# Kernel tuning notes

Measured on AMD Instinct MI355X. Metric: run time of the kernel, lower is better.

Reference implementation:

```python
import jax, jax.numpy as jnp
import numpy as np

N = 65536   # total nodes (B graphs * PG nodes)
B = 4096    # number of session graphs in batch
PG = 16     # nodes per graph
D = 128     # embedding_dim (= GRU hidden = attn hidden)
MAXD = 8    # max in-degree (mailbox length)
EPS = 1e-5  # BatchNorm eps


def _bn(x, gamma, beta, mean, var):
    # eval-mode BatchNorm1d
    return (x - mean) * (gamma / jnp.sqrt(var + EPS)) + beta


def _gru_cell(m, h, w_ih, w_hh, b_ih, b_hh):
    # torch.nn.GRU cell math; m,h: [N,D]
    gi = m @ w_ih.T + b_ih
    gh = h @ w_hh.T + b_hh
    i_r, i_z, i_n = jnp.split(gi, 3, axis=-1)
    h_r, h_z, h_n = jnp.split(gh, 3, axis=-1)
    r = jax.nn.sigmoid(i_r + h_r)
    z = jax.nn.sigmoid(i_z + h_z)
    n = jnp.tanh(i_n + r * h_n)
    return (1.0 - z) * n + z * h


def _forward(feat, intend, position_weight,
             bn1_gamma, bn1_beta, bn1_mean, bn1_var,
             gru_w_ih, gru_w_hh, gru_b_ih, gru_b_hh,
             fc_self_w, fc_neigh_w, prelu_a,
             bn2_gamma, bn2_beta, bn2_mean, bn2_var,
             fc_u_w, fc_v_w, fc_v_b, fc_i_w, fc_i_b, fc_e_w,
             last_nodes, edge_src, edge_dst, edge_slot, seg_ids):
    # ---- EOPA: copy_u messages -> per-node GRU over mailbox -> final hidden ----
    x = _bn(feat, bn1_gamma, bn1_beta, bn1_mean, bn1_var)
    mailbox = jnp.zeros((N, MAXD, D), x.dtype).at[edge_dst, edge_slot].set(x[edge_src])
    mask = jnp.zeros((N, MAXD), bool).at[edge_dst, edge_slot].set(True)

    def step(h, inp):
        m_t, mk_t = inp  # [N,D], [N]
        h_new = _gru_cell(m_t, h, gru_w_ih, gru_w_hh, gru_b_ih, gru_b_hh)
        return jnp.where(mk_t[:, None], h_new, h), None

    h0 = jnp.zeros((N, D), x.dtype)
    neigh, _ = jax.lax.scan(step, h0, (mailbox.transpose(1, 0, 2), mask.T))
    rst = x @ fc_self_w.T + neigh @ fc_neigh_w.T
    rst = jnp.where(rst > 0, rst, prelu_a * rst)  # PReLU(embedding_dim)

    # ---- AttnReadout: segment softmax attention + position-weighted readout ----
    f = _bn(rst, bn2_gamma, bn2_beta, bn2_mean, bn2_var)
    feat_u = f @ fc_u_w.T                                  # [N,D]
    feat_v = (intend @ fc_v_w.T + fc_v_b)[seg_ids]         # broadcast_nodes
    feat_l = (f[last_nodes] @ fc_i_w.T + fc_i_b)[seg_ids]  # broadcast_nodes
    e = (jax.nn.sigmoid(feat_u + feat_v + feat_l) @ fc_e_w.T)[:, 0]  # [N]
    # segment softmax over graphs
    e_max = jax.ops.segment_max(e, seg_ids, num_segments=B)
    e_exp = jnp.exp(e - e_max[seg_ids])
    denom = jax.ops.segment_sum(e_exp, seg_ids, num_segments=B)
    alpha = e_exp / denom[seg_ids]
    rst_g = jax.ops.segment_sum(f * alpha[:, None], seg_ids, num_segments=B)
    pos_g = jax.ops.segment_sum(f * position_weight[:, None], seg_ids, num_segments=B)
    return rst_g, pos_g


def setup_inputs() -> dict:
    rng = np.random.default_rng(0)
    deg = rng.integers(1, 5, size=N)                    # in-degree 1..4 <= MAXD
    E = int(deg.sum())
    edge_dst = np.repeat(np.arange(N), deg).astype(np.int32)
    starts = np.concatenate([[0], np.cumsum(deg)[:-1]])
    edge_slot = (np.arange(E) - np.repeat(starts, deg)).astype(np.int32)
    graph_of = (np.arange(N) // PG).astype(np.int32)
    edge_src = (graph_of[edge_dst].astype(np.int64) * PG
                + rng.integers(0, PG, size=E)).astype(np.int32)
    last_nodes = (np.arange(B) * PG + PG - 1).astype(np.int32)

    key = jax.random.key(0)
    ks = jax.random.split(key, 20)
    s = 0.05
    nrm = lambda k, sh, sc=s: jax.random.normal(k, sh, dtype=jnp.float32) * sc
    return dict(
        feat=nrm(ks[0], (N, D), 1.0),
        intend=nrm(ks[1], (B, D), 1.0),
        position_weight=jax.random.uniform(ks[2], (N,), dtype=jnp.float32),
        bn1_gamma=jnp.ones((D,), jnp.float32), bn1_beta=jnp.zeros((D,), jnp.float32),
        bn1_mean=nrm(ks[3], (D,)), bn1_var=jnp.ones((D,), jnp.float32),
        gru_w_ih=nrm(ks[4], (3 * D, D)), gru_w_hh=nrm(ks[5], (3 * D, D)),
        gru_b_ih=nrm(ks[6], (3 * D,)), gru_b_hh=nrm(ks[7], (3 * D,)),
        fc_self_w=nrm(ks[8], (D, D)), fc_neigh_w=nrm(ks[9], (D, D)),
        prelu_a=jnp.full((D,), 0.25, jnp.float32),
        bn2_gamma=jnp.ones((D,), jnp.float32), bn2_beta=jnp.zeros((D,), jnp.float32),
        bn2_mean=nrm(ks[10], (D,)), bn2_var=jnp.ones((D,), jnp.float32),
        fc_u_w=nrm(ks[11], (D, D)), fc_v_w=nrm(ks[12], (D, D)), fc_v_b=nrm(ks[13], (D,)),
        fc_i_w=nrm(ks[14], (D, D)), fc_i_b=nrm(ks[15], (D,)),
        fc_e_w=nrm(ks[16], (1, D)),
        last_nodes=jnp.asarray(last_nodes),
        edge_src=jnp.asarray(edge_src), edge_dst=jnp.asarray(edge_dst),
        edge_slot=jnp.asarray(edge_slot), seg_ids=jnp.asarray(graph_of),
    )


def reference(feat, intend, position_weight,
              bn1_gamma, bn1_beta, bn1_mean, bn1_var,
              gru_w_ih, gru_w_hh, gru_b_ih, gru_b_hh,
              fc_self_w, fc_neigh_w, prelu_a,
              bn2_gamma, bn2_beta, bn2_mean, bn2_var,
              fc_u_w, fc_v_w, fc_v_b, fc_i_w, fc_i_b, fc_e_w,
              last_nodes, edge_src, edge_dst, edge_slot, seg_ids):
    return _forward(feat, intend, position_weight,
                    bn1_gamma, bn1_beta, bn1_mean, bn1_var,
                    gru_w_ih, gru_w_hh, gru_b_ih, gru_b_hh,
                    fc_self_w, fc_neigh_w, prelu_a,
                    bn2_gamma, bn2_beta, bn2_mean, bn2_var,
                    fc_u_w, fc_v_w, fc_v_b, fc_i_w, fc_i_b, fc_e_w,
                    last_nodes, edge_src, edge_dst, edge_slot, seg_ids)
```

## Files before the change

kernel.cpp:

```cpp
#include <hip/hip_runtime.h>
#include <math.h>

#define D 128
#define MAXD 8
#define EPSV 1e-5f

#define NODES 32
#define NI 2

typedef __attribute__((ext_vector_type(8))) short short8;
typedef __attribute__((ext_vector_type(4))) float f32x4;
typedef unsigned short ushort_t;

#define XH_OFF     0
#define RZ_OFF     8192
#define RZ_STRIDE  132
#define NP_OFF     25088
#define NP_STRIDE  68
#define X2_OFF     NP_OFF
#define F_OFF      RZ_OFF
#define SBIG_BYTES 33792

__device__ __forceinline__ float fast_rcp(float x) { return __builtin_amdgcn_rcpf(x); }
__device__ __forceinline__ float sigmoid_f(float x) {
    return fast_rcp(1.0f + __expf(-x));
}
__device__ __forceinline__ float tanh_f(float x) {
    return 1.0f - 2.0f * fast_rcp(1.0f + __expf(2.0f * x));
}
__device__ __forceinline__ ushort_t f2bf(float f) {
    unsigned int b = __float_as_uint(f);
    b += 0x7FFFu + ((b >> 16) & 1u);
    return (ushort_t)(b >> 16);
}
__device__ __forceinline__ float bf2f(ushort_t u) {
    return __uint_as_float(((unsigned int)u) << 16);
}

__global__ void prep_kernel(const float* __restrict__ wih, const float* __restrict__ whh,
                            const float* __restrict__ fs,  const float* __restrict__ fn,
                            const float* __restrict__ fu,  const float* __restrict__ fv,
                            const float* __restrict__ fi,
                            const float* __restrict__ g1, const float* __restrict__ b1,
                            const float* __restrict__ m1, const float* __restrict__ v1,
                            ushort_t* __restrict__ wih_bf, ushort_t* __restrict__ whh_bf,
                            ushort_t* __restrict__ fcs_bf, ushort_t* __restrict__ fcn_bf,
                            ushort_t* __restrict__ fcu_bf, ushort_t* __restrict__ fcv_bf,
                            ushort_t* __restrict__ fci_bf,
                            float* __restrict__ bn1sc, float* __restrict__ bn1sh) {
    int i = blockIdx.x * blockDim.x + threadIdx.x;
    if (i < 3 * D * D) {
        wih_bf[i] = f2bf(wih[i]);
        whh_bf[i] = f2bf(whh[i]);
    }
    if (i < D * D) {
        fcs_bf[i] = f2bf(fs[i]);
        fcn_bf[i] = f2bf(fn[i]);
        fcu_bf[i] = f2bf(fu[i]);
        fcv_bf[i] = f2bf(fv[i]);
        fci_bf[i] = f2bf(fi[i]);
    }
    if (i < D) {
        float sc = g1[i] * rsqrtf(v1[i] + EPSV);
        bn1sc[i] = sc;
        bn1sh[i] = b1[i] - m1[i] * sc;
    }
}

__global__ void mbinit_kernel(int* __restrict__ mb, int n) {
    int i = blockIdx.x * blockDim.x + threadIdx.x;
    if (i < n) mb[i] = -1;
}
__global__ void scatter_kernel(const int* __restrict__ src, const int* __restrict__ dst,
                               const int* __restrict__ slot, int* __restrict__ mb, int E) {
    int e = blockIdx.x * blockDim.x + threadIdx.x;
    if (e < E) mb[(size_t)dst[e] * MAXD + slot[e]] = src[e];
}

__device__ __forceinline__ void stage_bn1(const float* __restrict__ feat,
                                          const float* __restrict__ bn1sc,
                                          const float* __restrict__ bn1sh,
                                          int node0, int tid, char* dst) {
    int row = tid >> 4, u = tid & 15;
    const float4* fp = (const float4*)(feat + (size_t)(node0 + row) * D + u * 8);
    const float4* scp = (const float4*)(bn1sc + u * 8);
    const float4* shp = (const float4*)(bn1sh + u * 8);
    float4 f0 = fp[0], f1 = fp[1];
    float4 s0 = scp[0], s1 = scp[1];
    float4 h0 = shp[0], h1 = shp[1];
    unsigned int w0 = (unsigned int)f2bf(f0.x * s0.x + h0.x) | ((unsigned int)f2bf(f0.y * s0.y + h0.y) << 16);
    unsigned int w1 = (unsigned int)f2bf(f0.z * s0.z + h0.z) | ((unsigned int)f2bf(f0.w * s0.w + h0.w) << 16);
    unsigned int w2 = (unsigned int)f2bf(f1.x * s1.x + h1.x) | ((unsigned int)f2bf(f1.y * s1.y + h1.y) << 16);
    unsigned int w3 = (unsigned int)f2bf(f1.z * s1.z + h1.z) | ((unsigned int)f2bf(f1.w * s1.w + h1.w) << 16);
    *(uint4*)(dst + row * 256 + ((u ^ (row & 7)) << 4)) = make_uint4(w0, w1, w2, w3);
}

__global__ __launch_bounds__(512, 2) void mega_kernel(
        const float* __restrict__ feat, const int* __restrict__ mb,
        const ushort_t* __restrict__ wih_bf, const ushort_t* __restrict__ whh_bf,
        const float* __restrict__ gbih, const float* __restrict__ gbhh,
        const ushort_t* __restrict__ fcs_bf, const ushort_t* __restrict__ fcn_bf,
        const float* __restrict__ prelu,
        const float* __restrict__ bg, const float* __restrict__ bb,
        const float* __restrict__ bm, const float* __restrict__ bv,
        const ushort_t* __restrict__ fcu_bf, const ushort_t* __restrict__ fcv_bf,
        const ushort_t* __restrict__ fci_bf,
        const float* __restrict__ fvbias, const float* __restrict__ fibias,
        const float* __restrict__ fce,
        const float* __restrict__ intend, const float* __restrict__ pw,
        const float* __restrict__ bn1sc, const float* __restrict__ bn1sh,
        float* __restrict__ outp, int Bn) {
    __shared__ __align__(16) char sBig[SBIG_BYTES];
    __shared__ int   sSrcT[MAXD][36];
    __shared__ float sE[NODES][9];
    __shared__ float sAlpha[NODES];
    __shared__ float sPw[NODES];
    __shared__ int   sTmax;

    const int tid = threadIdx.x;
    const int w = tid >> 6;
    const int lane = tid & 63;
    const int lc = lane & 15;
    const int lg = lane >> 4;
    const int c = w * 16 + lc;
    const int node0 = blockIdx.x * NODES;
    const int g0 = blockIdx.x * (NODES / 16);

    const int swzc = c >> 3;
    const int clo = (c & 7) * 2;

    if (tid == 0) sTmax = 0;
    stage_bn1(feat, bn1sc, bn1sh, node0, tid, sBig + XH_OFF);
    if (tid < NODES * MAXD) {
        int rr = tid >> 3, ss = tid & 7;
        int s = mb[(size_t)(node0 + rr) * MAXD + ss];
        sSrcT[ss][rr] = (s >= 0) ? (s - node0) : -1;
    }
    if (tid < NODES) sPw[tid] = pw[node0 + tid];
    __syncthreads();
    if (tid < NODES) {
        int d = 0;
#pragma unroll
        for (int t = 0; t < MAXD; ++t)
            if (sSrcT[t][tid] >= 0) d = t + 1;
        atomicMax(&sTmax, d);
    }

    {
        short8 bIW[3][4];
#pragma unroll
        for (int g = 0; g < 3; ++g)
#pragma unroll
            for (int kf = 0; kf < 4; ++kf)
                bIW[g][kf] = *(const short8*)(wih_bf + (size_t)(g * D + c) * D + kf * 32 + lg * 8);
        const float bi0 = gbih[c], bi1 = gbih[D + c], bi2 = gbih[2 * D + c];

#pragma unroll
        for (int i = 0; i < NI; ++i) {
            int xrow = i * 16 + lc;
            short8 aF[4];
#pragma unroll
            for (int kf = 0; kf < 4; ++kf)
                aF[kf] = *(const short8*)(sBig + XH_OFF + xrow * 256 + (((kf * 4 + lg) ^ (xrow & 7)) << 4));
            f32x4 aR = {0.f, 0.f, 0.f, 0.f}, aZ = aR, aN = aR;
#pragma unroll
            for (int kf = 0; kf < 4; ++kf) {
                aR = __builtin_amdgcn_mfma_f32_16x16x32_bf16(aF[kf], bIW[0][kf], aR, 0, 0, 0);
                aZ = __builtin_amdgcn_mfma_f32_16x16x32_bf16(aF[kf], bIW[1][kf], aZ, 0, 0, 0);
                aN = __builtin_amdgcn_mfma_f32_16x16x32_bf16(aF[kf], bIW[2][kf], aN, 0, 0, 0);
            }
#pragma unroll
            for (int p = 0; p < 4; ++p) {
                int row = i * 16 + lg * 4 + p;
                unsigned int rz = (unsigned int)f2bf(aR[p] + bi0)
                                | ((unsigned int)f2bf(aZ[p] + bi1) << 16);
                *(unsigned int*)(sBig + RZ_OFF + c * RZ_STRIDE + row * 4) = rz;
                *(ushort_t*)(sBig + NP_OFF + c * NP_STRIDE + row * 2) = f2bf(aN[p] + bi2);
            }
            __builtin_amdgcn_sched_barrier(0);
        }
    }
    __syncthreads();

    const int Tmax = (sTmax > 0) ? sTmax : 1;
    short8 bHW[3][4];
#pragma unroll
    for (int g = 0; g < 3; ++g)
#pragma unroll
        for (int kf = 0; kf < 4; ++kf)
            bHW[g][kf] = *(const short8*)(whh_bf + (size_t)(g * D + c) * D + kf * 32 + lg * 8);
    const float bhr = gbhh[c], bhz = gbhh[D + c], bhn = gbhh[2 * D + c];

    for (int t = 0; t < Tmax; ++t) {
        unsigned int houts[NI][2];
#pragma unroll
        for (int i = 0; i < NI; ++i) {
            f32x4 aR = {0.f, 0.f, 0.f, 0.f}, aZ = aR, aHN = aR;
            if (t != 0) {
                int hrow = i * 16 + lc;
                short8 aF[4];
#pragma unroll
                for (int kf = 0; kf < 4; ++kf)
                    aF[kf] = *(const short8*)(sBig + XH_OFF + hrow * 256 + (((kf * 4 + lg) ^ (hrow & 7)) << 4));
#pragma unroll
                for (int kf = 0; kf < 4; ++kf) {
                    aR  = __builtin_amdgcn_mfma_f32_16x16x32_bf16(aF[kf], bHW[0][kf], aR, 0, 0, 0);
                    aZ  = __builtin_amdgcn_mfma_f32_16x16x32_bf16(aF[kf], bHW[1][kf], aZ, 0, 0, 0);
                    aHN = __builtin_amdgcn_mfma_f32_16x16x32_bf16(aF[kf], bHW[2][kf], aHN, 0, 0, 0);
                }
            }
#pragma unroll
            for (int p = 0; p < 4; ++p) {
                int row = i * 16 + lg * 4 + p;
                int srow = sSrcT[t][row];
                int act = srow >= 0;
                int gr = act ? srow : 0;
                unsigned int rz = *(const unsigned int*)(sBig + RZ_OFF + c * RZ_STRIDE + gr * 4);
                float gir = bf2f((ushort_t)(rz & 0xffffu));
                float giz = bf2f((ushort_t)(rz >> 16));
                float gin = bf2f(*(const ushort_t*)(sBig + NP_OFF + c * NP_STRIDE + gr * 2));
                float hold = 0.0f;
                if (t != 0)
                    hold = bf2f(*(const ushort_t*)(sBig + XH_OFF + row * 256 + ((swzc ^ (row & 7)) << 4) + clo));
                float r = sigmoid_f(gir + aR[p] + bhr);
                float z = sigmoid_f(giz + aZ[p] + bhz);
                float n = tanh_f(gin + r * (aHN[p] + bhn));
                float hv = (1.0f - z) * n + z * hold;
                hv = act ? hv : hold;
                unsigned int hb = (unsigned int)f2bf(hv);
                if (p & 1) houts[i][p >> 1] |= hb << 16;
                else       houts[i][p >> 1]  = hb;
            }
            __builtin_amdgcn_sched_barrier(0);
        }
        __syncthreads();
#pragma unroll
        for (int i = 0; i < NI; ++i)
#pragma unroll
            for (int p = 0; p < 4; ++p) {
                int row = i * 16 + lg * 4 + p;
                ushort_t hb = (ushort_t)((houts[i][p >> 1] >> ((p & 1) * 16)) & 0xffffu);
                *(ushort_t*)(sBig + XH_OFF + row * 256 + ((swzc ^ (row & 7)) << 4) + clo) = hb;
            }
        __syncthreads();
    }

    stage_bn1(feat, bn1sc, bn1sh, node0, tid, sBig + X2_OFF);
    __syncthreads();
    {
        const float pa = prelu[c];
        const float s2 = bg[c] * rsqrtf(bv[c] + EPSV);
        const float h2 = bb[c] - bm[c] * s2;
        const ushort_t* fcs_c = fcs_bf + (size_t)c * D + lg * 8;
        const ushort_t* fcn_c = fcn_bf + (size_t)c * D + lg * 8;
#pragma unroll
        for (int i = 0; i < NI; ++i) {
            int xrow = i * 16 + lc;
            f32x4 a = {0.f, 0.f, 0.f, 0.f};
            {
                short8 xA[4];
#pragma unroll
                for (int kf = 0; kf < 4; ++kf)
                    xA[kf] = *(const short8*)(sBig + X2_OFF + xrow * 256 + (((kf * 4 + lg) ^ (xrow & 7)) << 4));
#pragma unroll
                for (int kf = 0; kf < 4; ++kf)
                    a = __builtin_amdgcn_mfma_f32_16x16x32_bf16(xA[kf], *(const short8*)(fcs_c + kf * 32), a, 0, 0, 0);
            }
            {
                short8 hA[4];
#pragma unroll
                for (int kf = 0; kf < 4; ++kf)
                    hA[kf] = *(const short8*)(sBig + XH_OFF + xrow * 256 + (((kf * 4 + lg) ^ (xrow & 7)) << 4));
#pragma unroll
                for (int kf = 0; kf < 4; ++kf)
                    a = __builtin_amdgcn_mfma_f32_16x16x32_bf16(hA[kf], *(const short8*)(fcn_c + kf * 32), a, 0, 0, 0);
            }
#pragma unroll
            for (int p = 0; p < 4; ++p) {
                int row = i * 16 + lg * 4 + p;
                float v = a[p];
                v = v > 0.0f ? v : pa * v;
                v = v * s2 + h2;
                *(ushort_t*)(sBig + F_OFF + row * 256 + ((swzc ^ (row & 7)) << 4) + clo) = f2bf(v);
            }
            __builtin_amdgcn_sched_barrier(0);
        }
    }
    __syncthreads();

    {
        const ushort_t* fcu_c = fcu_bf + (size_t)c * D + lg * 8;
        const ushort_t* fcv_c = fcv_bf + (size_t)c * D + lg * 8;
        const ushort_t* fci_c = fci_bf + (size_t)c * D + lg * 8;
        f32x4 vl4 = {0.f, 0.f, 0.f, 0.f};
        {
            int vrow = g0 + (lc & 1);
#pragma unroll
            for (int kf = 0; kf < 4; ++kf) {
                const float* ip = intend + (size_t)vrow * D + kf * 32 + lg * 8;
                float4 a0 = ((const float4*)ip)[0], a1 = ((const float4*)ip)[1];
                union { short8 v; ushort_t u[8]; } av;
                av.u[0] = f2bf(a0.x); av.u[1] = f2bf(a0.y); av.u[2] = f2bf(a0.z); av.u[3] = f2bf(a0.w);
                av.u[4] = f2bf(a1.x); av.u[5] = f2bf(a1.y); av.u[6] = f2bf(a1.z); av.u[7] = f2bf(a1.w);
                vl4 = __builtin_amdgcn_mfma_f32_16x16x32_bf16(av.v, *(const short8*)(fcv_c + kf * 32), vl4, 0, 0, 0);
            }
            int lrow = (lc & 1) * 16 + 15;
#pragma unroll
            for (int kf = 0; kf < 4; ++kf) {
                short8 al = *(const short8*)(sBig + F_OFF + lrow * 256 + (((kf * 4 + lg) ^ (lrow & 7)) << 4));
                vl4 = __builtin_amdgcn_mfma_f32_16x16x32_bf16(al, *(const short8*)(fci_c + kf * 32), vl4, 0, 0, 0);
            }
        }
        const float vbias = fvbias[c] + fibias[c];
        float vl_b[4];
#pragma unroll
        for (int p = 0; p < 4; ++p) vl_b[p] = vl4[p] + vbias;
        const float fcec = fce[c];

#pragma unroll
        for (int i = 0; i < NI; ++i) {
            int frow = i * 16 + lc;
            f32x4 u4 = {0.f, 0.f, 0.f, 0.f};
#pragma unroll
            for (int kf = 0; kf < 4; ++kf) {
                short8 af = *(const short8*)(sBig + F_OFF + frow * 256 + (((kf * 4 + lg) ^ (frow & 7)) << 4));
                u4 = __builtin_amdgcn_mfma_f32_16x16x32_bf16(af, *(const short8*)(fcu_c + kf * 32), u4, 0, 0, 0);
            }
            float vli = __shfl(vl_b[i & 3], lc, 64);
#pragma unroll
            for (int p = 0; p < 4; ++p) {
                float ev = sigmoid_f(u4[p] + vli) * fcec;
                ev += __shfl_xor(ev, 1);
                ev += __shfl_xor(ev, 2);
                ev += __shfl_xor(ev, 4);
                ev += __shfl_xor(ev, 8);
                if (lc == 0) sE[i * 16 + lg * 4 + p][w] = ev;
            }
            __builtin_amdgcn_sched_barrier(0);
        }
    }
    __syncthreads();

    if (tid < NODES) {
        float e = 0.0f;
#pragma unroll
        for (int q = 0; q < 8; ++q) e += sE[tid][q];
        float mx = e;
        mx = fmaxf(mx, __shfl_xor(mx, 1));
        mx = fmaxf(mx, __shfl_xor(mx, 2));
        mx = fmaxf(mx, __shfl_xor(mx, 4));
        mx = fmaxf(mx, __shfl_xor(mx, 8));
        float ex = __expf(e - mx);
        float sm = ex;
        sm += __shfl_xor(sm, 1);
        sm += __shfl_xor(sm, 2);
        sm += __shfl_xor(sm, 4);
        sm += __shfl_xor(sm, 8);
        sAlpha[tid] = ex * fast_rcp(sm);
    }
    __syncthreads();

#pragma unroll
    for (int i = 0; i < NI; ++i) {
        float ra = 0.0f, pb = 0.0f;
#pragma unroll
        for (int p = 0; p < 4; ++p) {
            int row = i * 16 + lg * 4 + p;
            float fv = bf2f(*(const ushort_t*)(sBig + F_OFF + row * 256 + ((swzc ^ (row & 7)) << 4) + clo));
            ra = fmaf(sAlpha[row], fv, ra);
            pb = fmaf(sPw[row],    fv, pb);
        }
        ra += __shfl_xor(ra, 16);
        ra += __shfl_xor(ra, 32);
        pb += __shfl_xor(pb, 16);
        pb += __shfl_xor(pb, 32);
        if (lg == 0) {
            outp[(size_t)(g0 + i) * D + c] = ra;
            outp[(size_t)Bn * D + (size_t)(g0 + i) * D + c] = pb;
        }
    }
}

extern "C" void kernel_launch(void* const* d_in, const int* in_sizes, int n_in,
                              void* d_out, int out_size, void* d_ws, size_t ws_size,
                              hipStream_t stream) {
    const float* feat   = (const float*)d_in[0];
    const float* intend = (const float*)d_in[1];
    const float* posw   = (const float*)d_in[2];
    const float* bn1g   = (const float*)d_in[3];
    const float* bn1b   = (const float*)d_in[4];
    const float* bn1m   = (const float*)d_in[5];
    const float* bn1v   = (const float*)d_in[6];
    const float* gwih   = (const float*)d_in[7];
    const float* gwhh   = (const float*)d_in[8];
    const float* gbih   = (const float*)d_in[9];
    const float* gbhh   = (const float*)d_in[10];
    const float* fcs    = (const float*)d_in[11];
    const float* fcn    = (const float*)d_in[12];
    const float* prelu  = (const float*)d_in[13];
    const float* bn2g   = (const float*)d_in[14];
    const float* bn2b   = (const float*)d_in[15];
    const float* bn2m   = (const float*)d_in[16];
    const float* bn2v   = (const float*)d_in[17];
    const float* fcu    = (const float*)d_in[18];
    const float* fcv    = (const float*)d_in[19];
    const float* fcvb   = (const float*)d_in[20];
    const float* fci    = (const float*)d_in[21];
    const float* fcib   = (const float*)d_in[22];
    const float* fce    = (const float*)d_in[23];
    const int* esrc     = (const int*)d_in[25];
    const int* edst     = (const int*)d_in[26];
    const int* eslot    = (const int*)d_in[27];

    const int N = in_sizes[0] / D;
    const int B = in_sizes[1] / D;
    const int E = in_sizes[25];

    char* wsb = (char*)d_ws;
    ushort_t* wih_bf = (ushort_t*)wsb;
    ushort_t* whh_bf = wih_bf + 3 * D * D;
    ushort_t* fcs_bf = whh_bf + 3 * D * D;
    ushort_t* fcn_bf = fcs_bf + D * D;
    ushort_t* fcu_bf = fcn_bf + D * D;
    ushort_t* fcv_bf = fcu_bf + D * D;
    ushort_t* fci_bf = fcv_bf + D * D;
    float* bn1sc = (float*)(fci_bf + D * D);
    float* bn1sh = bn1sc + D;
    int*   mb    = (int*)(bn1sh + D);

    prep_kernel<<<(3 * D * D + 255) / 256, 256, 0, stream>>>(
        gwih, gwhh, fcs, fcn, fcu, fcv, fci,
        bn1g, bn1b, bn1m, bn1v,
        wih_bf, whh_bf, fcs_bf, fcn_bf, fcu_bf, fcv_bf, fci_bf, bn1sc, bn1sh);
    mbinit_kernel<<<(N * MAXD + 255) / 256, 256, 0, stream>>>(mb, N * MAXD);
    scatter_kernel<<<(E + 255) / 256, 256, 0, stream>>>(esrc, edst, eslot, mb, E);
    mega_kernel<<<N / NODES, 512, 0, stream>>>(
        feat, mb, wih_bf, whh_bf, gbih, gbhh, fcs_bf, fcn_bf,
        prelu, bn2g, bn2b, bn2m, bn2v,
        fcu_bf, fcv_bf, fci_bf, fcvb, fcib, fce,
        intend, posw, bn1sc, bn1sh, (float*)d_out, B);
}
```

Measured before the change: 135.5 us.

## Double-buffer GRU hidden state in LDS and keep fp32 hidden in registers

Adds two ping-pong hidden-state buffers in shared memory so each GRU step reads from one and writes to the other. This drops the second __syncthreads and the separate write-back phase per step. The old hidden value now stays in fp32 registers instead of being re-read from LDS as bf16. LDS use grows by about 8 KB per block, which may lower occupancy. The sched_barrier is also removed.

```diff
diff --git a/kernel.cpp b/kernel.cpp
--- a/kernel.cpp
+++ b/kernel.cpp
@@ -12,14 +12,15 @@
 typedef __attribute__((ext_vector_type(4))) float f32x4;
 typedef unsigned short ushort_t;
 
-#define XH_OFF     0
-#define RZ_OFF     8192
+#define HB0_OFF    0
+#define HB1_OFF    8192
+#define RZ_OFF     16384
 #define RZ_STRIDE  132
-#define NP_OFF     25088
+#define NP_OFF     33280
 #define NP_STRIDE  68
 #define X2_OFF     NP_OFF
 #define F_OFF      RZ_OFF
-#define SBIG_BYTES 33792
+#define SBIG_BYTES 41984
 
 __device__ __forceinline__ float fast_rcp(float x) { return __builtin_amdgcn_rcpf(x); }
 __device__ __forceinline__ float sigmoid_f(float x) {
@@ -130,7 +131,7 @@
     const int clo = (c & 7) * 2;
 
     if (tid == 0) sTmax = 0;
-    stage_bn1(feat, bn1sc, bn1sh, node0, tid, sBig + XH_OFF);
+    stage_bn1(feat, bn1sc, bn1sh, node0, tid, sBig + HB0_OFF);
     if (tid < NODES * MAXD) {
         int rr = tid >> 3, ss = tid & 7;
         int s = mb[(size_t)(node0 + rr) * MAXD + ss];
@@ -161,7 +162,7 @@
             short8 aF[4];
 #pragma unroll
             for (int kf = 0; kf < 4; ++kf)
-                aF[kf] = *(const short8*)(sBig + XH_OFF + xrow * 256 + (((kf * 4 + lg) ^ (xrow & 7)) << 4));
+                aF[kf] = *(const short8*)(sBig + HB0_OFF + xrow * 256 + (((kf * 4 + lg) ^ (xrow & 7)) << 4));
             f32x4 aR = {0.f, 0.f, 0.f, 0.f}, aZ = aR, aN = aR;
 #pragma unroll
             for (int kf = 0; kf < 4; ++kf) {
@@ -191,8 +192,15 @@
             bHW[g][kf] = *(const short8*)(whh_bf + (size_t)(g * D + c) * D + kf * 32 + lg * 8);
     const float bhr = gbhh[c], bhz = gbhh[D + c], bhn = gbhh[2 * D + c];
 
+    float hreg[NI][4];
+#pragma unroll
+    for (int i = 0; i < NI; ++i)
+#pragma unroll
+        for (int p = 0; p < 4; ++p) hreg[i][p] = 0.0f;
+
     for (int t = 0; t < Tmax; ++t) {
-        unsigned int houts[NI][2];
+        const int rb = ((t + 1) & 1) ? HB1_OFF : HB0_OFF;
+        const int wb = (t & 1) ? HB1_OFF : HB0_OFF;
 #pragma unroll
         for (int i = 0; i < NI; ++i) {
             f32x4 aR = {0.f, 0.f, 0.f, 0.f}, aZ = aR, aHN = aR;
@@ -201,7 +209,7 @@
                 short8 aF[4];
 #pragma unroll
                 for (int kf = 0; kf < 4; ++kf)
-                    aF[kf] = *(const short8*)(sBig + XH_OFF + hrow * 256 + (((kf * 4 + lg) ^ (hrow & 7)) << 4));
+                    aF[kf] = *(const short8*)(sBig + rb + hrow * 256 + (((kf * 4 + lg) ^ (hrow & 7)) << 4));
 #pragma unroll
                 for (int kf = 0; kf < 4; ++kf) {
                     aR  = __builtin_amdgcn_mfma_f32_16x16x32_bf16(aF[kf], bHW[0][kf], aR, 0, 0, 0);
@@ -219,31 +227,17 @@
                 float gir = bf2f((ushort_t)(rz & 0xffffu));
                 float giz = bf2f((ushort_t)(rz >> 16));
                 float gin = bf2f(*(const ushort_t*)(sBig + NP_OFF + c * NP_STRIDE + gr * 2));
-                float hold = 0.0f;
-                if (t != 0)
-                    hold = bf2f(*(const ushort_t*)(sBig + XH_OFF + row * 256 + ((swzc ^ (row & 7)) << 4) + clo));
                 float r = sigmoid_f(gir + aR[p] + bhr);
                 float z = sigmoid_f(giz + aZ[p] + bhz);
                 float n = tanh_f(gin + r * (aHN[p] + bhn));
-                float hv = (1.0f - z) * n + z * hold;
-                hv = act ? hv : hold;
-                unsigned int hb = (unsigned int)f2bf(hv);
-                if (p & 1) houts[i][p >> 1] |= hb << 16;
-                else       houts[i][p >> 1]  = hb;
-            }
-            __builtin_amdgcn_sched_barrier(0);
+                float hv = (1.0f - z) * n + z * hreg[i][p];
+                hreg[i][p] = act ? hv : hreg[i][p];
+                *(ushort_t*)(sBig + wb + row * 256 + ((swzc ^ (row & 7)) << 4) + clo) = f2bf(hreg[i][p]);
+            }
         }
         __syncthreads();
-#pragma unroll
-        for (int i = 0; i < NI; ++i)
-#pragma unroll
-            for (int p = 0; p < 4; ++p) {
-                int row = i * 16 + lg * 4 + p;
-                ushort_t hb = (ushort_t)((houts[i][p >> 1] >> ((p & 1) * 16)) & 0xffffu);
-                *(ushort_t*)(sBig + XH_OFF + row * 256 + ((swzc ^ (row & 7)) << 4) + clo) = hb;
-            }
-        __syncthreads();
-    }
+    }
+    const int hb = ((Tmax - 1) & 1) ? HB1_OFF : HB0_OFF;
 
     stage_bn1(feat, bn1sc, bn1sh, node0, tid, sBig + X2_OFF);
     __syncthreads();
@@ -270,7 +264,7 @@
                 short8 hA[4];
 #pragma unroll
                 for (int kf = 0; kf < 4; ++kf)
-                    hA[kf] = *(const short8*)(sBig + XH_OFF + xrow * 256 + (((kf * 4 + lg) ^ (xrow & 7)) << 4));
+                    hA[kf] = *(const short8*)(sBig + hb + xrow * 256 + (((kf * 4 + lg) ^ (xrow & 7)) << 4));
 #pragma unroll
                 for (int kf = 0; kf < 4; ++kf)
                     a = __builtin_amdgcn_mfma_f32_16x16x32_bf16(hA[kf], *(const short8*)(fcn_c + kf * 32), a, 0, 0, 0);
```

Result: slower. 185.4 us (+36.8%).
